# Kernel tuning notes

Hardware: AMD Instinct MI355X
Metric: run time of the kernel (lower is better)

## Reference

```python
import jax, jax.numpy as jnp
import numpy as np
from jax import lax

DT, TAU = 16.67, 40.0
ALPHA = DT / TAU
ONE_MINUS_ALPHA = 1.0 - ALPHA


def setup_inputs() -> dict:
    key = jax.random.key(0)
    k = jax.random.split(key, 6)
    B, T, D, H = 256, 2048, 32, 64
    x = jax.random.normal(k[0], (B, T, D), dtype=jnp.float32)
    seq_lengths = jax.random.randint(k[1], (B,), 0, T, dtype=jnp.int32)
    W_in = jax.random.normal(k[2], (H, D), dtype=jnp.float32) * (1.0 / np.sqrt(D))
    b_in = jax.random.normal(k[3], (H,), dtype=jnp.float32) * 0.01
    W_hh = jax.random.normal(k[4], (H, H), dtype=jnp.float32) * (1.0 / np.sqrt(H))
    b_hh = jax.random.normal(k[5], (H,), dtype=jnp.float32) * 0.01
    return {"x": x, "seq_lengths": seq_lengths, "W_in": W_in, "b_in": b_in,
            "W_hh": W_hh, "b_hh": b_hh}


def reference(x, seq_lengths, W_in, b_in, W_hh, b_hh):
    B, T, D = x.shape
    H = W_hh.shape[0]
    # mask[b, t] = (t < seq_lengths[b]); forward value is identical either way
    # (the torch masking only stops gradients past seq end).
    mask = (jnp.arange(T)[None, :] < seq_lengths[:, None]).astype(x.dtype)  # [B,T]
    # Precompute input projection for all timesteps in one GEMM: [B,T,H]
    x_proj = jnp.einsum('btd,hd->bth', x, W_in) + b_in
    h0 = jnp.zeros((B, H), dtype=x.dtype)

    def step(h, inp):
        xp_t, m_t = inp  # [B,H], [B,1]
        pre = xp_t + h @ W_hh.T + b_hh
        h_new = jax.nn.relu(h * ONE_MINUS_ALPHA + pre * ALPHA)
        # hidden*mask + detach(hidden)*(1-mask): same value, gradient gated by mask
        h_new = h_new * m_t + lax.stop_gradient(h_new) * (1.0 - m_t)
        return h_new, h_new

    xs = (jnp.transpose(x_proj, (1, 0, 2)), mask.T[:, :, None])  # time-major
    h_last, outs = lax.scan(step, h0, xs)
    outputs = jnp.transpose(outs, (1, 0, 2))  # [B,T,H]
    return outputs, h_last
```

## Files before the change

kernel.cpp:

```cpp
#include <hip/hip_runtime.h>


#define Bb 256
#define Tt 2048
#define Dd 32
#define Hh 64

typedef float v2f __attribute__((ext_vector_type(2)));
typedef float v4f __attribute__((ext_vector_type(4)));

static constexpr float ALPHA = (float)(16.67 / 40.0);
static constexpr float OMA   = 1.0f - ALPHA;

static __device__ inline v2f vfma2(v2f a, v2f b, v2f c) {
#if __has_builtin(__builtin_elementwise_fma)
    return __builtin_elementwise_fma(a, b, c);
#else
    v2f r; r.x = fmaf(a.x, b.x, c.x); r.y = fmaf(a.y, b.y, c.y); return r;
#endif
}

__global__ __launch_bounds__(256) void ctrnn_xproj(
    const float* __restrict__ x,
    const float* __restrict__ W_in,
    float* __restrict__ xq)
{
    __shared__ alignas(16) float xs[128 * Dd];
    const int tid  = threadIdx.x;
    const int lane = tid & 63;
    const int wave = tid >> 6;
    const int b    = blockIdx.x >> 4;
    const int tile = blockIdx.x & 15;
    const int t0   = tile * 128;

    const float4* xsrc = reinterpret_cast<const float4*>(
        x + (size_t)b * Tt * Dd + (size_t)t0 * Dd);
    float4* xdst = reinterpret_cast<float4*>(xs);
#pragma unroll
    for (int r = 0; r < 4; ++r) xdst[r * 256 + tid] = xsrc[r * 256 + tid];

    v2f w[16];
    const v2f* wrow = reinterpret_cast<const v2f*>(W_in + lane * Dd);
#pragma unroll
    for (int j = 0; j < 16; ++j) w[j] = wrow[j];

    __syncthreads();

    float* ob = xq + (size_t)b * Tt * Hh + (size_t)t0 * Hh;
    const int lt0 = wave * 32;
#pragma unroll 2
    for (int i = 0; i < 32; ++i) {
        const float4* xr = reinterpret_cast<const float4*>(xs + (lt0 + i) * Dd);
        v2f a01 = {0.f, 0.f}, a23 = {0.f, 0.f};
#pragma unroll
        for (int j = 0; j < 8; ++j) {
            const float4 xv = xr[j];
            const v2f x01 = {xv.x, xv.y};
            const v2f x23 = {xv.z, xv.w};
            a01 = vfma2(w[2 * j + 0], x01, a01);
            a23 = vfma2(w[2 * j + 1], x23, a23);
        }
        ob[(size_t)(lt0 + i) * Hh + lane] = (a01.x + a01.y) + (a23.x + a23.y);
    }
}

__global__ __launch_bounds__(64) void ctrnn_recur_ws(
    const float* __restrict__ b_in,
    const float* __restrict__ W_hh,
    const float* __restrict__ b_hh,
    const float* __restrict__ xq,
    float* __restrict__ out)
{
    const int b    = blockIdx.x;
    const int lane = threadIdx.x;

    __shared__ alignas(16) float hs[Hh];

    v4f w4[16];
    const v4f* wr = reinterpret_cast<const v4f*>(W_hh + lane * Hh);
#pragma unroll
    for (int j = 0; j < 16; ++j) w4[j] = wr[j];

    const float cb = ALPHA * (b_in[lane] + b_hh[lane]);

    const float* xb = xq + (size_t)b * Tt * Hh + lane;
    float*       op = out + (size_t)b * Tt * Hh + lane;

    float xp[8];
#pragma unroll
    for (int j = 0; j < 8; ++j) xp[j] = xb[(size_t)j * Hh];
    const float* lp = xb + 8 * (size_t)Hh;

    const v4f* h4 = reinterpret_cast<const v4f*>(hs);

    hs[lane] = 0.0f;
    v4f q0 = h4[8],  q1 = h4[9],  q2 = h4[10], q3 = h4[11];
    v4f q4 = h4[12], q5 = h4[13], q6 = h4[14], q7 = h4[15];

    float hold = 0.0f;
    float pre  = cb;
    for (int t = 0; t < Tt; t += 8) {
#pragma unroll
        for (int j = 0; j < 8; ++j) {
            const int hb = __float_as_int(hold);
            float s0 = 0.f, s1 = 0.f, s2 = 0.f, s3 = 0.f;
#pragma unroll
            for (int k = 0; k < 8; ++k) {
                const float h0 = __int_as_float(__builtin_amdgcn_readlane(hb, 4 * k + 0));
                const float h1 = __int_as_float(__builtin_amdgcn_readlane(hb, 4 * k + 1));
                const float h2 = __int_as_float(__builtin_amdgcn_readlane(hb, 4 * k + 2));
                const float h3 = __int_as_float(__builtin_amdgcn_readlane(hb, 4 * k + 3));
                s0 = fmaf(w4[k][0], h0, s0);
                s1 = fmaf(w4[k][1], h1, s1);
                s2 = fmaf(w4[k][2], h2, s2);
                s3 = fmaf(w4[k][3], h3, s3);
            }
            v2f acc01 = {s0, s1}, acc23 = {s2, s3};
#define QPK(K, Q)                                                              \
            acc01 = vfma2(__builtin_shufflevector(w4[K], w4[K], 0, 1),         \
                          __builtin_shufflevector((Q), (Q), 0, 1), acc01);     \
            acc23 = vfma2(__builtin_shufflevector(w4[K], w4[K], 2, 3),         \
                          __builtin_shufflevector((Q), (Q), 2, 3), acc23);
            QPK( 8, q0) QPK( 9, q1) QPK(10, q2) QPK(11, q3)
            QPK(12, q4) QPK(13, q5) QPK(14, q6) QPK(15, q7)
#undef QPK
            const v2f tt     = acc01 + acc23;
            const float sum  = (tt.x + tt.y) + xp[j];
            const float hnew = fmaxf(fmaf(ALPHA, sum, pre), 0.0f);

            hs[lane] = hnew;
            q0 = h4[8];  q1 = h4[9];  q2 = h4[10]; q3 = h4[11];
            q4 = h4[12]; q5 = h4[13]; q6 = h4[14]; q7 = h4[15];
            __builtin_amdgcn_sched_barrier(0);

            *op = hnew;
            op += Hh;
            hold = hnew;
            pre  = fmaf(OMA, hnew, cb);

            xp[j] = *lp;
            lp += Hh;
        }
    }
    out[(size_t)Bb * Tt * Hh + (size_t)b * Hh + lane] = hold;
}

__global__ __launch_bounds__(64) void ctrnn_recur_ip(
    const float* __restrict__ b_in,
    const float* __restrict__ W_hh,
    const float* __restrict__ b_hh,
    float* __restrict__ out)
{
    const int b    = blockIdx.x;
    const int lane = threadIdx.x;

    __shared__ alignas(16) float hs[Hh];

    float4 w4[16];
    const float4* wr = reinterpret_cast<const float4*>(W_hh + lane * Hh);
#pragma unroll
    for (int j = 0; j < 16; ++j) w4[j] = wr[j];

    const float cb = ALPHA * (b_in[lane] + b_hh[lane]);

    float* ob = out + (size_t)b * Tt * Hh + lane;

    float xp[8];
#pragma unroll
    for (int j = 0; j < 8; ++j) xp[j] = ob[(size_t)j * Hh];

    float* op       = ob;
    const float* lp = ob + 8 * (size_t)Hh;

    const float4* h4 = reinterpret_cast<const float4*>(hs);

    hs[lane] = 0.0f;
    float4 q0 = h4[8],  q1 = h4[9],  q2 = h4[10], q3 = h4[11];
    float4 q4 = h4[12], q5 = h4[13], q6 = h4[14], q7 = h4[15];

    float hold = 0.0f;
    for (int t = 0; t < Tt; t += 8) {
#pragma unroll
        for (int j = 0; j < 8; ++j) {
            const int hb = __float_as_int(hold);
            float s0 = 0.f, s1 = 0.f, s2 = 0.f, s3 = 0.f;
#pragma unroll
            for (int k = 0; k < 8; ++k) {
                const float h0 = __int_as_float(__builtin_amdgcn_readlane(hb, 4 * k + 0));
                const float h1 = __int_as_float(__builtin_amdgcn_readlane(hb, 4 * k + 1));
                const float h2 = __int_as_float(__builtin_amdgcn_readlane(hb, 4 * k + 2));
                const float h3 = __int_as_float(__builtin_amdgcn_readlane(hb, 4 * k + 3));
                s0 = fmaf(w4[k].x, h0, s0);
                s1 = fmaf(w4[k].y, h1, s1);
                s2 = fmaf(w4[k].z, h2, s2);
                s3 = fmaf(w4[k].w, h3, s3);
            }
            s0 = fmaf(w4[ 8].x, q0.x, s0); s1 = fmaf(w4[ 8].y, q0.y, s1);
            s2 = fmaf(w4[ 8].z, q0.z, s2); s3 = fmaf(w4[ 8].w, q0.w, s3);
            s0 = fmaf(w4[ 9].x, q1.x, s0); s1 = fmaf(w4[ 9].y, q1.y, s1);
            s2 = fmaf(w4[ 9].z, q1.z, s2); s3 = fmaf(w4[ 9].w, q1.w, s3);
            s0 = fmaf(w4[10].x, q2.x, s0); s1 = fmaf(w4[10].y, q2.y, s1);
            s2 = fmaf(w4[10].z, q2.z, s2); s3 = fmaf(w4[10].w, q2.w, s3);
            s0 = fmaf(w4[11].x, q3.x, s0); s1 = fmaf(w4[11].y, q3.y, s1);
            s2 = fmaf(w4[11].z, q3.z, s2); s3 = fmaf(w4[11].w, q3.w, s3);
            s0 = fmaf(w4[12].x, q4.x, s0); s1 = fmaf(w4[12].y, q4.y, s1);
            s2 = fmaf(w4[12].z, q4.z, s2); s3 = fmaf(w4[12].w, q4.w, s3);
            s0 = fmaf(w4[13].x, q5.x, s0); s1 = fmaf(w4[13].y, q5.y, s1);
            s2 = fmaf(w4[13].z, q5.z, s2); s3 = fmaf(w4[13].w, q5.w, s3);
            s0 = fmaf(w4[14].x, q6.x, s0); s1 = fmaf(w4[14].y, q6.y, s1);
            s2 = fmaf(w4[14].z, q6.z, s2); s3 = fmaf(w4[14].w, q6.w, s3);
            s0 = fmaf(w4[15].x, q7.x, s0); s1 = fmaf(w4[15].y, q7.y, s1);
            s2 = fmaf(w4[15].z, q7.z, s2); s3 = fmaf(w4[15].w, q7.w, s3);

            const float sum  = ((s0 + s2) + (s1 + s3)) + xp[j];
            const float hnew = fmaxf(fmaf(ALPHA, sum, fmaf(OMA, hold, cb)), 0.0f);

            hs[lane] = hnew;
            q0 = h4[8];  q1 = h4[9];  q2 = h4[10]; q3 = h4[11];
            q4 = h4[12]; q5 = h4[13]; q6 = h4[14]; q7 = h4[15];

            *op = hnew;
            op += Hh;
            hold = hnew;

            xp[j] = *lp;
            lp += Hh;
        }
    }
    out[(size_t)Bb * Tt * Hh + (size_t)b * Hh + lane] = hold;
}

extern "C" void kernel_launch(void* const* d_in, const int* in_sizes, int n_in,
                              void* d_out, int out_size, void* d_ws, size_t ws_size,
                              hipStream_t stream) {
    const float* x    = (const float*)d_in[0];
    const float* W_in = (const float*)d_in[2];
    const float* b_in = (const float*)d_in[3];
    const float* W_hh = (const float*)d_in[4];
    const float* b_hh = (const float*)d_in[5];
    float* out = (float*)d_out;

    const size_t need = ((size_t)Bb * Tt + 16) * (size_t)Hh * sizeof(float);
    if (d_ws != nullptr && ws_size >= need) {
        float* xq = (float*)d_ws;
        ctrnn_xproj<<<dim3(Bb * 16), dim3(256), 0, stream>>>(x, W_in, xq);
        ctrnn_recur_ws<<<dim3(Bb), dim3(64), 0, stream>>>(b_in, W_hh, b_hh, xq, out);
    } else {
        ctrnn_xproj<<<dim3(Bb * 16), dim3(256), 0, stream>>>(x, W_in, out);
        ctrnn_recur_ip<<<dim3(Bb), dim3(64), 0, stream>>>(b_in, W_hh, b_hh, out);
    }
}
```

Baseline: 537.7 us.

## Rebalance recurrence readlane/LDS split and register-prefetch x rows in projection

The projection kernel no longer stages x tiles through shared memory. Each wave now loads its rows straight into registers with double buffering, so the next row's loads overlap the current row's FMAs and the block barrier is gone. In the recurrent kernel, the h-vector split changes from 32 lanes via readlane plus 32 via LDS to 8 via readlane plus 56 via LDS, moving work off the serial scalar readlane path onto wide LDS loads. Launch bounds are raised to one block per SIMD to allow more registers, at the cost of more LDS traffic per step.

```diff
diff --git a/kernel.cpp b/kernel.cpp
--- a/kernel.cpp
+++ b/kernel.cpp
@@ -25,46 +25,55 @@
     const float* __restrict__ W_in,
     float* __restrict__ xq)
 {
-    __shared__ alignas(16) float xs[128 * Dd];
     const int tid  = threadIdx.x;
     const int lane = tid & 63;
     const int wave = tid >> 6;
     const int b    = blockIdx.x >> 4;
     const int tile = blockIdx.x & 15;
-    const int t0   = tile * 128;
-
-    const float4* xsrc = reinterpret_cast<const float4*>(
-        x + (size_t)b * Tt * Dd + (size_t)t0 * Dd);
-    float4* xdst = reinterpret_cast<float4*>(xs);
-#pragma unroll
-    for (int r = 0; r < 4; ++r) xdst[r * 256 + tid] = xsrc[r * 256 + tid];
+    const int r0   = tile * 128 + wave * 32;
 
     v2f w[16];
     const v2f* wrow = reinterpret_cast<const v2f*>(W_in + lane * Dd);
 #pragma unroll
     for (int j = 0; j < 16; ++j) w[j] = wrow[j];
 
-    __syncthreads();
-
-    float* ob = xq + (size_t)b * Tt * Hh + (size_t)t0 * Hh;
-    const int lt0 = wave * 32;
-#pragma unroll 2
-    for (int i = 0; i < 32; ++i) {
-        const float4* xr = reinterpret_cast<const float4*>(xs + (lt0 + i) * Dd);
-        v2f a01 = {0.f, 0.f}, a23 = {0.f, 0.f};
-#pragma unroll
-        for (int j = 0; j < 8; ++j) {
-            const float4 xv = xr[j];
-            const v2f x01 = {xv.x, xv.y};
-            const v2f x23 = {xv.z, xv.w};
-            a01 = vfma2(w[2 * j + 0], x01, a01);
-            a23 = vfma2(w[2 * j + 1], x23, a23);
-        }
-        ob[(size_t)(lt0 + i) * Hh + lane] = (a01.x + a01.y) + (a23.x + a23.y);
-    }
-}
-
-__global__ __launch_bounds__(64) void ctrnn_recur_ws(
+    const float4* base = reinterpret_cast<const float4*>(
+        x + (size_t)b * Tt * Dd + (size_t)r0 * Dd);
+    float* ob = xq + (size_t)b * Tt * Hh + (size_t)r0 * Hh;
+
+#define XROW(BUF, RIDX)                                                       \
+    {                                                                         \
+        v2f a01 = {0.f, 0.f}, a23 = {0.f, 0.f};                               \
+        _Pragma("unroll")                                                     \
+        for (int j = 0; j < 8; ++j) {                                         \
+            const float4 xv = (BUF)[j];                                       \
+            const v2f x01 = {xv.x, xv.y};                                     \
+            const v2f x23 = {xv.z, xv.w};                                     \
+            a01 = vfma2(w[2 * j + 0], x01, a01);                              \
+            a23 = vfma2(w[2 * j + 1], x23, a23);                              \
+        }                                                                     \
+        ob[(size_t)(RIDX) * Hh + lane] = (a01.x + a01.y) + (a23.x + a23.y);   \
+    }
+
+    float4 ba[8], bb[8];
+#pragma unroll
+    for (int j = 0; j < 8; ++j) ba[j] = base[j];
+
+    for (int i = 0; i < 32; i += 2) {
+        const float4* p1 = base + (size_t)(i + 1) * 8;
+#pragma unroll
+        for (int j = 0; j < 8; ++j) bb[j] = p1[j];
+        XROW(ba, i)
+        const int i2 = (i < 30) ? (i + 2) : 31;
+        const float4* p2 = base + (size_t)i2 * 8;
+#pragma unroll
+        for (int j = 0; j < 8; ++j) ba[j] = p2[j];
+        XROW(bb, i + 1)
+    }
+#undef XROW
+}
+
+__global__ __launch_bounds__(64, 1) void ctrnn_recur_ws(
     const float* __restrict__ b_in,
     const float* __restrict__ W_hh,
     const float* __restrict__ b_hh,
@@ -94,8 +103,10 @@
     const v4f* h4 = reinterpret_cast<const v4f*>(hs);
 
     hs[lane] = 0.0f;
-    v4f q0 = h4[8],  q1 = h4[9],  q2 = h4[10], q3 = h4[11];
-    v4f q4 = h4[12], q5 = h4[13], q6 = h4[14], q7 = h4[15];
+    v4f q0  = h4[2],  q1  = h4[3],  q2  = h4[4],  q3  = h4[5];
+    v4f q4  = h4[6],  q5  = h4[7],  q6  = h4[8],  q7  = h4[9];
+    v4f q8  = h4[10], q9  = h4[11], q10 = h4[12], q11 = h4[13];
+    v4f q12 = h4[14], q13 = h4[15];
 
     float hold = 0.0f;
     float pre  = cb;
@@ -105,7 +116,7 @@
             const int hb = __float_as_int(hold);
             float s0 = 0.f, s1 = 0.f, s2 = 0.f, s3 = 0.f;
 #pragma unroll
-            for (int k = 0; k < 8; ++k) {
+            for (int k = 0; k < 2; ++k) {
                 const float h0 = __int_as_float(__builtin_amdgcn_readlane(hb, 4 * k + 0));
                 const float h1 = __int_as_float(__builtin_amdgcn_readlane(hb, 4 * k + 1));
                 const float h2 = __int_as_float(__builtin_amdgcn_readlane(hb, 4 * k + 2));
@@ -121,16 +132,20 @@
                           __builtin_shufflevector((Q), (Q), 0, 1), acc01);     \
             acc23 = vfma2(__builtin_shufflevector(w4[K], w4[K], 2, 3),         \
                           __builtin_shufflevector((Q), (Q), 2, 3), acc23);
-            QPK( 8, q0) QPK( 9, q1) QPK(10, q2) QPK(11, q3)
-            QPK(12, q4) QPK(13, q5) QPK(14, q6) QPK(15, q7)
+            QPK( 2, q0)  QPK( 3, q1)  QPK( 4, q2)  QPK( 5, q3)
+            QPK( 6, q4)  QPK( 7, q5)  QPK( 8, q6)  QPK( 9, q7)
+            QPK(10, q8)  QPK(11, q9)  QPK(12, q10) QPK(13, q11)
+            QPK(14, q12) QPK(15, q13)
 #undef QPK
             const v2f tt     = acc01 + acc23;
             const float sum  = (tt.x + tt.y) + xp[j];
             const float hnew = fmaxf(fmaf(ALPHA, sum, pre), 0.0f);
 
             hs[lane] = hnew;
-            q0 = h4[8];  q1 = h4[9];  q2 = h4[10]; q3 = h4[11];
-            q4 = h4[12]; q5 = h4[13]; q6 = h4[14]; q7 = h4[15];
+            q0  = h4[2];  q1  = h4[3];  q2  = h4[4];  q3  = h4[5];
+            q4  = h4[6];  q5  = h4[7];  q6  = h4[8];  q7  = h4[9];
+            q8  = h4[10]; q9  = h4[11]; q10 = h4[12]; q11 = h4[13];
+            q12 = h4[14]; q13 = h4[15];
             __builtin_amdgcn_sched_barrier(0);
 
             *op = hnew;
```

After: 646.8 us. +20.3%, slower.
